# Kernel optimization log

Measured on AMD Instinct MI355X. Metric: run time of the kernel, lower is better.

Reference implementation:

```python
import jax, jax.numpy as jnp
import numpy as np

C = 256
C8 = C // 8  # 32
B, H, W = 4, 128, 128
PH = PW = 32  # adaptive pool output size


def setup_inputs() -> dict:
    key = jax.random.key(0)
    ks = jax.random.split(key, 8)
    query_feat = jax.random.normal(ks[0], (B, C, H, W), dtype=jnp.float32)
    key_value_feat = jax.random.normal(ks[1], (B, C, H, W), dtype=jnp.float32)
    s = 1.0 / np.sqrt(C)
    Wq = jax.random.normal(ks[2], (C8, C), dtype=jnp.float32) * s
    bq = jnp.zeros((C8,), dtype=jnp.float32)
    Wk = jax.random.normal(ks[3], (C8, C), dtype=jnp.float32) * s
    bk = jnp.zeros((C8,), dtype=jnp.float32)
    Wv = jax.random.normal(ks[4], (C, C), dtype=jnp.float32) * s
    bv = jnp.zeros((C,), dtype=jnp.float32)
    gamma = jnp.zeros((1,), dtype=jnp.float32)
    return {"query_feat": query_feat, "key_value_feat": key_value_feat,
            "Wq": Wq, "bq": bq, "Wk": Wk, "bk": bk, "Wv": Wv, "bv": bv,
            "gamma": gamma}


def _adaptive_avg_pool(x):
    # x: (B, C, H, W) with H % PH == 0, W % PW == 0 -> uniform mean pooling
    b, c, h, w = x.shape
    x = x.reshape(b, c, PH, h // PH, PW, w // PW)
    return x.mean(axis=(3, 5))  # (B, C, PH, PW)


def reference(query_feat, key_value_feat, Wq, bq, Wk, bk, Wv, bv, gamma):
    b, c, h, w = query_feat.shape
    hw = h * w
    L = PH * PW  # 1024 pooled kv positions

    # 1x1 conv == channel matmul
    q = jnp.einsum('bchw,oc->bohw', query_feat, Wq) + bq[None, :, None, None]
    proj_query = q.reshape(b, C8, hw).transpose(0, 2, 1)  # (B, HW, C8)

    pooled = _adaptive_avg_pool(key_value_feat)  # (B, C, 32, 32)
    k = jnp.einsum('bcpq,oc->bopq', pooled, Wk) + bk[None, :, None, None]
    proj_key = k.reshape(b, C8, L)  # (B, C8, L)
    v = jnp.einsum('bcpq,oc->bopq', pooled, Wv) + bv[None, :, None, None]
    proj_value = v.reshape(b, c, L)  # (B, C, L)

    energy = jnp.einsum('bnc,bcl->bnl', proj_query, proj_key)  # (B, HW, L)
    attention = jax.nn.softmax(energy, axis=-1)
    out = jnp.einsum('bcl,bnl->bcn', proj_value, attention)  # (B, C, HW)
    out = out.reshape(b, c, h, w)
    return gamma[0] * out + query_feat
```

## Files before the change

### kernel.cpp

```cpp
#include <hip/hip_runtime.h>
#include <hip/hip_bf16.h>

typedef __attribute__((ext_vector_type(8))) short short8;
typedef __attribute__((ext_vector_type(4))) float f32x4;

__device__ __forceinline__ unsigned short f2bf(float x) {
    unsigned int u = __float_as_uint(x);
    u += 0x7fffu + ((u >> 16) & 1u);
    return (unsigned short)(u >> 16);
}

#define SWZ(row, col) (((((col) >> 3) ^ ((row) & 15)) << 3) | ((col) & 7))

#define BAR_LDS() asm volatile("s_waitcnt lgkmcnt(0)\n\ts_barrier" ::: "memory")

__global__ __launch_bounds__(256) void k_pool(const float* __restrict__ kv,
                                              float* __restrict__ pooled) {
    int idx = blockIdx.x * 256 + threadIdx.x;
    int pw = idx & 31;
    int ph = (idx >> 5) & 31;
    int bc = idx >> 10;
    const f32x4* row = (const f32x4*)(kv + ((size_t)bc * 128 + ph * 4) * 128);
    float s = 0.f;
#pragma unroll
    for (int i = 0; i < 4; ++i) {
        f32x4 v = row[i * 32 + pw];
        s += v[0] + v[1] + v[2] + v[3];
    }
    pooled[idx] = s * (1.f / 16.f);
}

__global__ __launch_bounds__(256) void k_kvproj(const float* __restrict__ pooled,
        const float* __restrict__ Wk, const float* __restrict__ bk,
        const float* __restrict__ Wv, const float* __restrict__ bv,
        unsigned short* __restrict__ Ktb, unsigned short* __restrict__ Vb) {
    int t = threadIdx.x;
    int lane = t & 63;
    int og = __builtin_amdgcn_readfirstlane(t >> 6);
    int blk = blockIdx.x;
    int b  = blk / 288;
    int r  = blk - b * 288;
    int ot = r >> 4;
    int lt = r & 15;
    int l  = lt * 64 + lane;
    int u0 = ot * 16 + og * 4;
    bool isK = (ot < 2);
    const float* Wbase = isK ? (Wk + (size_t)u0 * 256) : (Wv + (size_t)(u0 - 32) * 256);
    const float* bias  = isK ? (bk + u0) : (bv + (u0 - 32));
    const float* psrc  = pooled + (size_t)b * 256 * 1024 + l;

    float acc[4];
#pragma unroll
    for (int j = 0; j < 4; ++j) acc[j] = bias[j];
    for (int c0 = 0; c0 < 256; c0 += 8) {
        float p[8];
#pragma unroll
        for (int i = 0; i < 8; ++i) p[i] = psrc[(size_t)(c0 + i) * 1024];
#pragma unroll
        for (int j = 0; j < 4; ++j) {
            f32x4 w0 = *(const f32x4*)(Wbase + j * 256 + c0);
            f32x4 w1 = *(const f32x4*)(Wbase + j * 256 + c0 + 4);
            acc[j] += w0[0] * p[0] + w0[1] * p[1] + w0[2] * p[2] + w0[3] * p[3]
                    + w1[0] * p[4] + w1[1] * p[5] + w1[2] * p[6] + w1[3] * p[7];
        }
    }
    if (isK) {
        unsigned int k0 = (unsigned int)f2bf(acc[0]) | ((unsigned int)f2bf(acc[1]) << 16);
        unsigned int k1 = (unsigned int)f2bf(acc[2]) | ((unsigned int)f2bf(acc[3]) << 16);
        uint2 pk = {k0, k1};
        *(uint2*)&Ktb[((size_t)(b * 1024 + l)) * 32 + u0] = pk;
    } else {
#pragma unroll
        for (int j = 0; j < 4; ++j)
            Vb[((size_t)(b * 256 + u0 - 32 + j)) * 1024 + l] = f2bf(acc[j]);
    }
}

__global__ __launch_bounds__(256) void k_qproj(const float* __restrict__ query,
        const float* __restrict__ Wq, const float* __restrict__ bq,
        unsigned short* __restrict__ Qfb) {
    int t = threadIdx.x;
    int ln = t & 63;
    int o0 = __builtin_amdgcn_readfirstlane((t >> 6) * 8);
    int b = blockIdx.x >> 8;
    int n = (blockIdx.x & 255) * 64 + ln;
    const float* src = query + (size_t)b * 4194304 + n;
    float acc[8];
#pragma unroll
    for (int j = 0; j < 8; ++j) acc[j] = bq[o0 + j];
    for (int c0 = 0; c0 < 256; c0 += 8) {
        float v[8];
#pragma unroll
        for (int i = 0; i < 8; ++i) v[i] = src[(size_t)(c0 + i) * 16384];
#pragma unroll
        for (int j = 0; j < 8; ++j) {
            f32x4 w0 = *(const f32x4*)&Wq[(o0 + j) * 256 + c0];
            f32x4 w1 = *(const f32x4*)&Wq[(o0 + j) * 256 + c0 + 4];
            acc[j] += w0[0] * v[0] + w0[1] * v[1] + w0[2] * v[2] + w0[3] * v[3]
                    + w1[0] * v[4] + w1[1] * v[5] + w1[2] * v[6] + w1[3] * v[7];
        }
    }
    short8 pk;
#pragma unroll
    for (int j = 0; j < 8; ++j) pk[j] = (short)f2bf(acc[j]);
    *(short8*)&Qfb[((size_t)b * 16384 + n) * 32 + o0] = pk;
}

__global__ __launch_bounds__(512, 4) void k_attn(const unsigned short* __restrict__ Qfb,
        const unsigned short* __restrict__ Ktb, const unsigned short* __restrict__ Vb,
        const float* __restrict__ query, const float* __restrict__ gamma,
        float* __restrict__ out) {
    __shared__ unsigned short Pb[2][64][128];
    float (*wsumL)[16][8] = (float(*)[16][8])Pb;

    int t = threadIdx.x;
    int lane = t & 63, wv = t >> 6;
    int quad = lane >> 4, nl = lane & 15;
    int b = blockIdx.x >> 8;
    int n0 = (blockIdx.x & 255) * 64;

    short8 qfrag[4];
#pragma unroll
    for (int qt = 0; qt < 4; ++qt)
        qfrag[qt] = *(const short8*)&Qfb[((size_t)b * 16384 + n0 + qt * 16 + nl) * 32 + quad * 8];

    f32x4 acc[4][2];
#pragma unroll
    for (int qt = 0; qt < 4; ++qt)
#pragma unroll
        for (int ct = 0; ct < 2; ++ct) { f32x4 z = {0.f, 0.f, 0.f, 0.f}; acc[qt][ct] = z; }
    float rsum[4] = {0.f, 0.f, 0.f, 0.f};

    const unsigned short* ktb = Ktb + (size_t)b * 1024 * 32;
    const unsigned short* vbb = Vb + (size_t)b * 256 * 1024;

#define S_PHASE(ch, bi, kf)                                                      \
    {                                                                            \
        int lloc = wv * 16;                                                      \
        _Pragma("unroll")                                                        \
        for (int qt = 0; qt < 4; ++qt) {                                         \
            f32x4 z = {0.f, 0.f, 0.f, 0.f};                                      \
            f32x4 s = __builtin_amdgcn_mfma_f32_16x16x32_bf16(kf, qfrag[qt], z, 0, 0, 0); \
            f32x4 p;                                                             \
            _Pragma("unroll")                                                    \
            for (int i = 0; i < 4; ++i) p[i] = __expf(s[i]);                     \
            rsum[qt] += p[0] + p[1] + p[2] + p[3];                               \
            unsigned int w0 = (unsigned int)f2bf(p[0]) | ((unsigned int)f2bf(p[1]) << 16); \
            unsigned int w1 = (unsigned int)f2bf(p[2]) | ((unsigned int)f2bf(p[3]) << 16); \
            uint2 pk = {w0, w1};                                                 \
            int prow = qt * 16 + nl;                                             \
            int pcol = lloc + quad * 4;                                          \
            *(uint2*)&Pb[bi][prow][SWZ(prow, pcol)] = pk;                        \
        }                                                                        \
    }

#define K_ADDR(ch) ((const short8*)&ktb[((size_t)((ch) * 128 + wv * 16 + nl)) * 32 + quad * 8])
#define V_ADDR(ch, ks, ct) ((const short8*)&vbb[(size_t)(wv * 32 + (ct) * 16 + nl) * 1024 + (ch) * 128 + (ks) * 32 + quad * 8])

    short8 kpre = *K_ADDR(0);
    short8 vpre[8];
#pragma unroll
    for (int ks = 0; ks < 4; ++ks)
#pragma unroll
        for (int ct = 0; ct < 2; ++ct)
            vpre[ks * 2 + ct] = *V_ADDR(0, ks, ct);
    S_PHASE(0, 0, kpre)
    BAR_LDS();

    for (int ch = 0; ch < 8; ++ch) {
        int bi = ch & 1;
        if (ch < 7) kpre = *K_ADDR(ch + 1);
#pragma unroll
        for (int ks = 0; ks < 4; ++ks) {
            int rcol = ((ks * 4 + quad) ^ nl) << 3;
            short8 af[4];
#pragma unroll
            for (int qt = 0; qt < 4; ++qt)
                af[qt] = *(const short8*)&Pb[bi][qt * 16 + nl][rcol];
#pragma unroll
            for (int ct = 0; ct < 2; ++ct) {
                short8 bf = vpre[ks * 2 + ct];
#pragma unroll
                for (int qt = 0; qt < 4; ++qt)
                    acc[qt][ct] = __builtin_amdgcn_mfma_f32_16x16x32_bf16(af[qt], bf, acc[qt][ct], 0, 0, 0);
            }
        }
        if (ch < 7) {
#pragma unroll
            for (int ks = 0; ks < 4; ++ks)
#pragma unroll
                for (int ct = 0; ct < 2; ++ct)
                    vpre[ks * 2 + ct] = *V_ADDR(ch + 1, ks, ct);
            S_PHASE(ch + 1, bi ^ 1, kpre)
        }
        BAR_LDS();
    }

#pragma unroll
    for (int qt = 0; qt < 4; ++qt) {
        float v = rsum[qt];
        v += __shfl_xor(v, 16);
        v += __shfl_xor(v, 32);
        if (lane < 16) wsumL[qt][nl][wv] = v;
    }
    __syncthreads();

    float inv[4][4];
#pragma unroll
    for (int qt = 0; qt < 4; ++qt)
#pragma unroll
        for (int r = 0; r < 4; ++r) {
            f32x4 s0 = *(const f32x4*)&wsumL[qt][quad * 4 + r][0];
            f32x4 s1 = *(const f32x4*)&wsumL[qt][quad * 4 + r][4];
            inv[qt][r] = 1.0f / (s0[0] + s0[1] + s0[2] + s0[3] +
                                 s1[0] + s1[1] + s1[2] + s1[3]);
        }

    float g0 = gamma[0];
    const float* qsrc = query + (size_t)b * 4194304;
    float* odst = out + (size_t)b * 4194304;
#pragma unroll
    for (int qt = 0; qt < 4; ++qt)
#pragma unroll
        for (int ct = 0; ct < 2; ++ct) {
            int c = wv * 32 + ct * 16 + nl;
            size_t base = (size_t)c * 16384 + n0 + qt * 16 + quad * 4;
            f32x4 qv = *(const f32x4*)(qsrc + base);
            f32x4 o;
#pragma unroll
            for (int r = 0; r < 4; ++r) o[r] = g0 * acc[qt][ct][r] * inv[qt][r] + qv[r];
            *(f32x4*)(odst + base) = o;
        }
}

extern "C" void kernel_launch(void* const* d_in, const int* in_sizes, int n_in,
                              void* d_out, int out_size, void* d_ws, size_t ws_size,
                              hipStream_t stream) {
    const float* query = (const float*)d_in[0];
    const float* kvf   = (const float*)d_in[1];
    const float* Wq    = (const float*)d_in[2];
    const float* bq    = (const float*)d_in[3];
    const float* Wk    = (const float*)d_in[4];
    const float* bk    = (const float*)d_in[5];
    const float* Wv    = (const float*)d_in[6];
    const float* bv    = (const float*)d_in[7];
    const float* gamma = (const float*)d_in[8];
    float* out = (float*)d_out;

    float* pooled       = (float*)d_ws;
    unsigned short* Ktb = (unsigned short*)(pooled + 1048576);
    unsigned short* Vb  = Ktb + 131072;
    unsigned short* Qfb = Vb + 1048576;

    k_pool  <<<dim3(4096), dim3(256), 0, stream>>>(kvf, pooled);
    k_kvproj<<<dim3(1152), dim3(256), 0, stream>>>(pooled, Wk, bk, Wv, bv, Ktb, Vb);
    k_qproj <<<dim3(1024), dim3(256), 0, stream>>>(query, Wq, bq, Qfb);
    k_attn  <<<dim3(1024), dim3(512), 0, stream>>>(Qfb, Ktb, Vb, query, gamma, out);
}
```

Baseline: 292.8 us.

## Interleave QK softmax quarters with PV MFMA slots in attention main loop

Restructures the chunk loop so that each PV accumulation slot is followed by one quarter of the next chunk's score/exp computation. V loads are split into two halves issued mid-iteration, and K is prefetched two chunks ahead. The last chunk is peeled into an epilogue. The goal is to overlap exp/bf16 packing and global loads with MFMA work and shorten dependency stalls, at the cost of more live registers and a larger unrolled body.

```diff
diff --git a/kernel.cpp b/kernel.cpp
--- a/kernel.cpp
+++ b/kernel.cpp
@@ -134,67 +134,92 @@
     const unsigned short* ktb = Ktb + (size_t)b * 1024 * 32;
     const unsigned short* vbb = Vb + (size_t)b * 256 * 1024;
 
-#define S_PHASE(ch, bi, kf)                                                      \
-    {                                                                            \
-        int lloc = wv * 16;                                                      \
-        _Pragma("unroll")                                                        \
-        for (int qt = 0; qt < 4; ++qt) {                                         \
-            f32x4 z = {0.f, 0.f, 0.f, 0.f};                                      \
-            f32x4 s = __builtin_amdgcn_mfma_f32_16x16x32_bf16(kf, qfrag[qt], z, 0, 0, 0); \
-            f32x4 p;                                                             \
-            _Pragma("unroll")                                                    \
-            for (int i = 0; i < 4; ++i) p[i] = __expf(s[i]);                     \
-            rsum[qt] += p[0] + p[1] + p[2] + p[3];                               \
-            unsigned int w0 = (unsigned int)f2bf(p[0]) | ((unsigned int)f2bf(p[1]) << 16); \
-            unsigned int w1 = (unsigned int)f2bf(p[2]) | ((unsigned int)f2bf(p[3]) << 16); \
-            uint2 pk = {w0, w1};                                                 \
-            int prow = qt * 16 + nl;                                             \
-            int pcol = lloc + quad * 4;                                          \
-            *(uint2*)&Pb[bi][prow][SWZ(prow, pcol)] = pk;                        \
-        }                                                                        \
-    }
-
 #define K_ADDR(ch) ((const short8*)&ktb[((size_t)((ch) * 128 + wv * 16 + nl)) * 32 + quad * 8])
 #define V_ADDR(ch, ks, ct) ((const short8*)&vbb[(size_t)(wv * 32 + (ct) * 16 + nl) * 1024 + (ch) * 128 + (ks) * 32 + quad * 8])
 
+#define S_QUARTER(qt, bi2, kf)                                                   \
+    {                                                                            \
+        f32x4 z = {0.f, 0.f, 0.f, 0.f};                                          \
+        f32x4 s = __builtin_amdgcn_mfma_f32_16x16x32_bf16(kf, qfrag[qt], z, 0, 0, 0); \
+        f32x4 p;                                                                 \
+        _Pragma("unroll")                                                        \
+        for (int i = 0; i < 4; ++i) p[i] = __expf(s[i]);                         \
+        rsum[qt] += p[0] + p[1] + p[2] + p[3];                                   \
+        unsigned int w0 = (unsigned int)f2bf(p[0]) | ((unsigned int)f2bf(p[1]) << 16); \
+        unsigned int w1 = (unsigned int)f2bf(p[2]) | ((unsigned int)f2bf(p[3]) << 16); \
+        uint2 pk = {w0, w1};                                                     \
+        int prow = qt * 16 + nl;                                                 \
+        int pcol = wv * 16 + quad * 4;                                           \
+        *(uint2*)&Pb[bi2][prow][SWZ(prow, pcol)] = pk;                           \
+    }
+
+#define PV_SLOT(ks, bi)                                                          \
+    {                                                                            \
+        int rcol = (((ks) * 4 + quad) ^ nl) << 3;                                \
+        short8 af[4];                                                            \
+        _Pragma("unroll")                                                        \
+        for (int qt = 0; qt < 4; ++qt)                                           \
+            af[qt] = *(const short8*)&Pb[bi][qt * 16 + nl][rcol];                \
+        _Pragma("unroll")                                                        \
+        for (int ct = 0; ct < 2; ++ct) {                                         \
+            short8 bf = vp[(ks) * 2 + ct];                                       \
+            _Pragma("unroll")                                                    \
+            for (int qt = 0; qt < 4; ++qt)                                       \
+                acc[qt][ct] = __builtin_amdgcn_mfma_f32_16x16x32_bf16(af[qt], bf, acc[qt][ct], 0, 0, 0); \
+        }                                                                        \
+    }
+
     short8 kpre = *K_ADDR(0);
-    short8 vpre[8];
+    short8 kpA  = *K_ADDR(1);
+    short8 vp[8];
 #pragma unroll
     for (int ks = 0; ks < 4; ++ks)
 #pragma unroll
         for (int ct = 0; ct < 2; ++ct)
-            vpre[ks * 2 + ct] = *V_ADDR(0, ks, ct);
-    S_PHASE(0, 0, kpre)
+            vp[ks * 2 + ct] = *V_ADDR(0, ks, ct);
+    S_QUARTER(0, 0, kpre)
+    S_QUARTER(1, 0, kpre)
+    S_QUARTER(2, 0, kpre)
+    S_QUARTER(3, 0, kpre)
     BAR_LDS();
 
-    for (int ch = 0; ch < 8; ++ch) {
-        int bi = ch & 1;
-        if (ch < 7) kpre = *K_ADDR(ch + 1);
-#pragma unroll
-        for (int ks = 0; ks < 4; ++ks) {
-            int rcol = ((ks * 4 + quad) ^ nl) << 3;
-            short8 af[4];
-#pragma unroll
-            for (int qt = 0; qt < 4; ++qt)
-                af[qt] = *(const short8*)&Pb[bi][qt * 16 + nl][rcol];
-#pragma unroll
-            for (int ct = 0; ct < 2; ++ct) {
-                short8 bf = vpre[ks * 2 + ct];
-#pragma unroll
-                for (int qt = 0; qt < 4; ++qt)
-                    acc[qt][ct] = __builtin_amdgcn_mfma_f32_16x16x32_bf16(af[qt], bf, acc[qt][ct], 0, 0, 0);
-            }
-        }
-        if (ch < 7) {
-#pragma unroll
-            for (int ks = 0; ks < 4; ++ks)
-#pragma unroll
-                for (int ct = 0; ct < 2; ++ct)
-                    vpre[ks * 2 + ct] = *V_ADDR(ch + 1, ks, ct);
-            S_PHASE(ch + 1, bi ^ 1, kpre)
-        }
+    for (int ch = 0; ch < 7; ++ch) {
+        int bi = ch & 1, bi2 = bi ^ 1;
+        int chn = ch + 1;
+        int chk = (ch + 2 < 7) ? ch + 2 : 7;
+        short8 kpB = *K_ADDR(chk);
+
+        PV_SLOT(0, bi)
+        S_QUARTER(0, bi2, kpA)
+
+        PV_SLOT(1, bi)
+        S_QUARTER(1, bi2, kpA)
+        vp[0] = *V_ADDR(chn, 0, 0);
+        vp[1] = *V_ADDR(chn, 0, 1);
+        vp[2] = *V_ADDR(chn, 1, 0);
+        vp[3] = *V_ADDR(chn, 1, 1);
+
+        PV_SLOT(2, bi)
+        S_QUARTER(2, bi2, kpA)
+
+        PV_SLOT(3, bi)
+        S_QUARTER(3, bi2, kpA)
+        vp[4] = *V_ADDR(chn, 2, 0);
+        vp[5] = *V_ADDR(chn, 2, 1);
+        vp[6] = *V_ADDR(chn, 3, 0);
+        vp[7] = *V_ADDR(chn, 3, 1);
+
+        kpA = kpB;
         BAR_LDS();
     }
+    {
+        int bi = 1;
+        PV_SLOT(0, bi)
+        PV_SLOT(1, bi)
+        PV_SLOT(2, bi)
+        PV_SLOT(3, bi)
+    }
+    __syncthreads();
 
 #pragma unroll
     for (int qt = 0; qt < 4; ++qt) {
```

New measurement: 305.5 us. 4.3% more time.
